# Optimization experiments

Measured on AMD Instinct MI355X. Metric: run time of the kernel, lower is better.

## Reference

```python
import jax, jax.numpy as jnp
import numpy as np

N_EXPERTS = 16
IN_DIM = 1024
OUT_DIM = 1024
BATCH = 4096

def setup_inputs() -> dict:
    key = jax.random.key(0)
    k1, k2, k3, k4 = jax.random.split(key, 4)
    x = jax.random.normal(k1, (BATCH, IN_DIM), dtype=jnp.float32)
    comp_weight = jax.random.uniform(k2, (BATCH, N_EXPERTS), dtype=jnp.float32)
    # torch.rand init (uniform [0,1)) per original module
    weight = jax.random.uniform(k3, (N_EXPERTS, IN_DIM, OUT_DIM), dtype=jnp.float32)
    bias = jax.random.uniform(k4, (N_EXPERTS, OUT_DIM), dtype=jnp.float32)
    return {"x": x, "comp_weight": comp_weight, "weight": weight, "bias": bias}

def reference(x, comp_weight, weight, bias):
    # z[n,b,o] = x[b,i] @ weight[n,i,o] + bias[n,o]   (baddbmm)
    z = jnp.einsum('bi,nio->nbo', x, weight) + bias[:, None, :]
    # out[b,o] = sum_n comp_weight[b,n] * z[n,b,o]    (bmm combine)
    out = jnp.einsum('bn,nbo->bo', comp_weight, z)
    return jax.nn.relu(out)
```

## Files before the change

kernel.cpp:

```cpp
#include <hip/hip_runtime.h>
#include <hip/hip_bf16.h>
#include <cstdint>

#define BATCH   4096
#define IN_DIM  1024
#define OUT_DIM 1024
#define NEXP    16

typedef __bf16 bf16;
typedef __attribute__((ext_vector_type(8))) __bf16 bf16x8;
typedef __attribute__((ext_vector_type(4))) float  f32x4;

#define AS1 __attribute__((address_space(1)))
#define AS3 __attribute__((address_space(3)))

__device__ __forceinline__ void gld_lds16(const bf16* g, bf16* l) {
    __builtin_amdgcn_global_load_lds((const AS1 void*)g, (AS3 void*)l, 16, 0, 0);
}

__global__ __launch_bounds__(256) void convert_all(
        const float* __restrict__ x, const float* __restrict__ W,
        bf16* __restrict__ xt, bf16* __restrict__ wt) {
    __shared__ float Ls[64][65];
    int t = threadIdx.x;
    int bid = blockIdx.x;
    if (bid < 4096) {
        int nblk = bid >> 8, ne = (bid >> 4) & 15, ks = bid & 15;
        int kb = ne * 1024 + ks * 64;
        int n0 = nblk * 64;
#pragma unroll
        for (int r = 0; r < 4; r++) {
            int idx = r * 256 + t;
            int row = idx >> 4, c4 = (idx & 15) * 4;
            f32x4 v = *(const f32x4*)(W + (size_t)(kb + row) * OUT_DIM + n0 + c4);
#pragma unroll
            for (int j = 0; j < 4; j++) Ls[row][c4 + j] = v[j];
        }
        __syncthreads();
#pragma unroll
        for (int r = 0; r < 2; r++) {
            int c = r * 256 + t;
            int sub = c >> 6, l = c & 63;
            int lr = l & 15, lq = l >> 4;
            int kk = sub >> 2, wn = (sub >> 1) & 1, nt = sub & 1;
            int krow = kk * 32 + lq * 8;
            int col = wn * 32 + nt * 16 + lr;
            bf16x8 v;
#pragma unroll
            for (int j = 0; j < 8; j++) v[j] = (bf16)Ls[krow + j][col];
            *(bf16x8*)(wt + (size_t)bid * 4096 + c * 8) = v;
        }
    } else {
        int tile = bid - 4096;
        int mblk = tile >> 4, ks = tile & 15;
#pragma unroll
        for (int r = 0; r < 4; r++) {
            int q = r * 256 + t;
            int m_loc = q >> 3, sc = q & 7;
            int cc = sc ^ (m_loc & 7);
            const float* src = x + (size_t)(mblk * 128 + m_loc) * IN_DIM + ks * 64 + cc * 8;
            f32x4 a = *(const f32x4*)src;
            f32x4 b = *(const f32x4*)(src + 4);
            bf16x8 v;
#pragma unroll
            for (int j = 0; j < 4; j++) { v[j] = (bf16)a[j]; v[4 + j] = (bf16)b[j]; }
            *(bf16x8*)(xt + (size_t)tile * 8192 + q * 8) = v;
        }
    }
}

__global__ __launch_bounds__(256, 3) void moe_gemm(
        const float* __restrict__ cw, const float* __restrict__ bias,
        const bf16* __restrict__ xt, const bf16* __restrict__ wt,
        float* __restrict__ out) {
    int nblk = blockIdx.x;
    int mblk = blockIdx.y;
    int m0 = mblk * 128, n0 = nblk * 64;
    int t = threadIdx.x;
    int lane = t & 63, w = t >> 6;
    int wm = w >> 1, wn = w & 1;
    int lq = lane >> 4, lr = lane & 15;

    __shared__ bf16 As[128 * 64];
    __shared__ bf16 Bs[4][64 * 64];
    __shared__ float cwT[16 * 132];

#pragma unroll
    for (int r = 0; r < 2; r++) {
        int q = r * 256 + t;
        f32x4 v = *(const f32x4*)(cw + (size_t)m0 * NEXP + q * 4);
        int row = q >> 2, nb = (q & 3) * 4;
#pragma unroll
        for (int c2 = 0; c2 < 4; c2++) cwT[(nb + c2) * 132 + row] = v[c2];
    }

    const f32x4 fz = {0.f, 0.f, 0.f, 0.f};
    f32x4 acc[4][2];
#pragma unroll
    for (int mt = 0; mt < 4; mt++)
#pragma unroll
        for (int nt = 0; nt < 2; nt++) acc[mt][nt] = fz;

    int swz = lr & 7;
    int mrow[4];
#pragma unroll
    for (int mt = 0; mt < 4; mt++) mrow[mt] = (wm * 64 + mt * 16 + lr) * 64;

    const bf16* abase = xt + (size_t)(mblk * 16) * 8192;
    const bf16* bbase = wt + (size_t)nblk * (16 * 16 * 4096);

    for (int ks = 0; ks < 16; ks++) {
        const bf16* asrc = abase + (size_t)ks * 8192 + t * 8;
#pragma unroll
        for (int r = 0; r < 4; r++) gld_lds16(asrc + r * 2048, &As[r * 2048 + t * 8]);
        const bf16* b0 = bbase + (size_t)ks * 4096 + t * 8;
        gld_lds16(b0,        &Bs[0][t * 8]);
        gld_lds16(b0 + 2048, &Bs[0][2048 + t * 8]);
        const bf16* b1 = bbase + (size_t)(16 + ks) * 4096 + t * 8;
        gld_lds16(b1,        &Bs[1][t * 8]);
        gld_lds16(b1 + 2048, &Bs[1][2048 + t * 8]);
        __syncthreads();

        bf16x8 af[4][2];
#pragma unroll
        for (int kk = 0; kk < 2; kk++)
#pragma unroll
            for (int mt = 0; mt < 4; mt++)
                af[mt][kk] = *(const bf16x8*)&As[mrow[mt] + ((kk * 4 + lq) ^ swz) * 8];

#pragma unroll 2
        for (int s = 0; s < 8; s++) {
            int nbase = s * 2;
            if (s < 7) {
                const bf16* bn2 = bbase + (size_t)((nbase + 2) * 16 + ks) * 4096 + t * 8;
                bf16* bd2 = &Bs[(nbase + 2) & 3][t * 8];
                gld_lds16(bn2,        bd2);
                gld_lds16(bn2 + 2048, bd2 + 2048);
                const bf16* bn3 = bbase + (size_t)((nbase + 3) * 16 + ks) * 4096 + t * 8;
                bf16* bd3 = &Bs[(nbase + 3) & 3][t * 8];
                gld_lds16(bn3,        bd3);
                gld_lds16(bn3 + 2048, bd3 + 2048);
            }
#pragma unroll
            for (int e = 0; e < 2; e++) {
                int ne = nbase + e;
                bf16x8 bfr[2][2];
#pragma unroll
                for (int kk = 0; kk < 2; kk++)
#pragma unroll
                    for (int nt = 0; nt < 2; nt++)
                        bfr[kk][nt] = *(const bf16x8*)
                            &Bs[ne & 3][((kk * 2 + wn) * 2 + nt) * 512 + lane * 8];
                f32x4 sc[4];
#pragma unroll
                for (int mt = 0; mt < 4; mt++)
                    sc[mt] = *(const f32x4*)&cwT[ne * 132 + wm * 64 + mt * 16 + lq * 4];
#pragma unroll
                for (int mt = 0; mt < 4; mt++)
#pragma unroll
                    for (int nt = 0; nt < 2; nt++) {
                        f32x4 p = __builtin_amdgcn_mfma_f32_16x16x32_bf16(
                            af[mt][0], bfr[0][nt], fz, 0, 0, 0);
                        p = __builtin_amdgcn_mfma_f32_16x16x32_bf16(
                            af[mt][1], bfr[1][nt], p, 0, 0, 0);
                        acc[mt][nt] += sc[mt] * p;
                    }
            }
            __syncthreads();
        }
    }

    {
        bf16x8 acw[4];
#pragma unroll
        for (int mt = 0; mt < 4; mt++) {
            bf16x8 v;
#pragma unroll
            for (int j = 0; j < 8; j++) v[j] = (bf16)0.f;
            if (lq < 2) {
                int row = m0 + wm * 64 + mt * 16 + lr;
                f32x4 a = *(const f32x4*)(cw + (size_t)row * NEXP + lq * 8);
                f32x4 b = *(const f32x4*)(cw + (size_t)row * NEXP + lq * 8 + 4);
#pragma unroll
                for (int j = 0; j < 4; j++) { v[j] = (bf16)a[j]; v[4 + j] = (bf16)b[j]; }
            }
            acw[mt] = v;
        }
        bf16x8 bb[2];
#pragma unroll
        for (int nt = 0; nt < 2; nt++) {
            bf16x8 v;
#pragma unroll
            for (int j = 0; j < 8; j++) v[j] = (bf16)0.f;
            if (lq < 2) {
                int col = n0 + wn * 32 + nt * 16 + lr;
#pragma unroll
                for (int j = 0; j < 8; j++)
                    v[j] = (bf16)bias[(size_t)(lq * 8 + j) * OUT_DIM + col];
            }
            bb[nt] = v;
        }
#pragma unroll
        for (int mt = 0; mt < 4; mt++)
#pragma unroll
            for (int nt = 0; nt < 2; nt++)
                acc[mt][nt] = __builtin_amdgcn_mfma_f32_16x16x32_bf16(
                    acw[mt], bb[nt], acc[mt][nt], 0, 0, 0);
    }

#pragma unroll
    for (int mt = 0; mt < 4; mt++) {
        int row = m0 + wm * 64 + mt * 16 + lq * 4;
#pragma unroll
        for (int nt = 0; nt < 2; nt++) {
            int col = n0 + wn * 32 + nt * 16 + lr;
#pragma unroll
            for (int r2 = 0; r2 < 4; r2++) {
                float v = acc[mt][nt][r2];
                out[(size_t)(row + r2) * OUT_DIM + col] = v > 0.f ? v : 0.f;
            }
        }
    }
}

__global__ void fallback_kernel(const float* __restrict__ x, const float* __restrict__ cw,
                                const float* __restrict__ W, const float* __restrict__ bias,
                                float* __restrict__ out) {
    int o = blockIdx.x * 256 + threadIdx.x;
    int b = o >> 10, oc = o & 1023;
    const float* xr = x + (size_t)b * IN_DIM;
    float accv = 0.f;
    for (int n = 0; n < NEXP; n++) {
        const float* wr = W + (size_t)n * IN_DIM * OUT_DIM + oc;
        float z = 0.f;
        for (int i = 0; i < IN_DIM; i++) z += xr[i] * wr[(size_t)i * OUT_DIM];
        accv += cw[(size_t)b * NEXP + n] * (z + bias[n * OUT_DIM + oc]);
    }
    out[o] = accv > 0.f ? accv : 0.f;
}

extern "C" void kernel_launch(void* const* d_in, const int* in_sizes, int n_in,
                              void* d_out, int out_size, void* d_ws, size_t ws_size,
                              hipStream_t stream) {
    const float* x    = (const float*)d_in[0];
    const float* cw   = (const float*)d_in[1];
    const float* W    = (const float*)d_in[2];
    const float* bias = (const float*)d_in[3];
    float* out = (float*)d_out;

    const size_t wt_elems = (size_t)NEXP * IN_DIM * OUT_DIM;
    const size_t xt_elems = (size_t)BATCH * IN_DIM;
    if (ws_size < (wt_elems + xt_elems) * sizeof(bf16)) {
        fallback_kernel<<<(BATCH * OUT_DIM) / 256, 256, 0, stream>>>(x, cw, W, bias, out);
        return;
    }
    bf16* wt = (bf16*)d_ws;
    bf16* xt = wt + wt_elems;

    convert_all<<<4096 + 512, 256, 0, stream>>>(x, W, xt, wt);
    moe_gemm<<<dim3(16, 32), 256, 0, stream>>>(cw, bias, xt, wt, out);
}
```

Before: 260.2 us.

## Transpose MFMA operands so per-row expert scales live in registers

Swaps the A and B operands of the MFMA so each lane's accumulator holds one row and four consecutive columns. This lets the per-row gating weights be loaded once into registers as scalars, replacing the LDS-transposed cw table, and lets the output be written with 16-byte vector stores. The expert loop is fully unrolled and launch bounds drop to 2 waves per SIMD to give room for the 64 extra scale registers. The risk is lower occupancy and more code size from the full unroll.

```diff
diff --git a/kernel.cpp b/kernel.cpp
--- a/kernel.cpp
+++ b/kernel.cpp
@@ -69,7 +69,7 @@
     }
 }
 
-__global__ __launch_bounds__(256, 3) void moe_gemm(
+__global__ __launch_bounds__(256, 2) void moe_gemm(
         const float* __restrict__ cw, const float* __restrict__ bias,
         const bf16* __restrict__ xt, const bf16* __restrict__ wt,
         float* __restrict__ out) {
@@ -83,15 +83,13 @@
 
     __shared__ bf16 As[128 * 64];
     __shared__ bf16 Bs[4][64 * 64];
-    __shared__ float cwT[16 * 132];
-
-#pragma unroll
-    for (int r = 0; r < 2; r++) {
-        int q = r * 256 + t;
-        f32x4 v = *(const f32x4*)(cw + (size_t)m0 * NEXP + q * 4);
-        int row = q >> 2, nb = (q & 3) * 4;
-#pragma unroll
-        for (int c2 = 0; c2 < 4; c2++) cwT[(nb + c2) * 132 + row] = v[c2];
+
+    f32x4 sreg[4][4];
+#pragma unroll
+    for (int mt = 0; mt < 4; mt++) {
+        const f32x4* p = (const f32x4*)(cw + (size_t)(m0 + wm * 64 + mt * 16 + lr) * NEXP);
+#pragma unroll
+        for (int g = 0; g < 4; g++) sreg[mt][g] = p[g];
     }
 
     const f32x4 fz = {0.f, 0.f, 0.f, 0.f};
@@ -109,6 +107,7 @@
     const bf16* abase = xt + (size_t)(mblk * 16) * 8192;
     const bf16* bbase = wt + (size_t)nblk * (16 * 16 * 4096);
 
+#pragma unroll 1
     for (int ks = 0; ks < 16; ks++) {
         const bf16* asrc = abase + (size_t)ks * 8192 + t * 8;
 #pragma unroll
@@ -128,45 +127,38 @@
             for (int mt = 0; mt < 4; mt++)
                 af[mt][kk] = *(const bf16x8*)&As[mrow[mt] + ((kk * 4 + lq) ^ swz) * 8];
 
-#pragma unroll 2
-        for (int s = 0; s < 8; s++) {
-            int nbase = s * 2;
-            if (s < 7) {
-                const bf16* bn2 = bbase + (size_t)((nbase + 2) * 16 + ks) * 4096 + t * 8;
-                bf16* bd2 = &Bs[(nbase + 2) & 3][t * 8];
+#pragma unroll
+        for (int ne = 0; ne < 16; ne++) {
+            if ((ne & 1) == 0 && ne < 14) {
+                const bf16* bn2 = bbase + (size_t)((ne + 2) * 16 + ks) * 4096 + t * 8;
+                bf16* bd2 = &Bs[(ne + 2) & 3][t * 8];
                 gld_lds16(bn2,        bd2);
                 gld_lds16(bn2 + 2048, bd2 + 2048);
-                const bf16* bn3 = bbase + (size_t)((nbase + 3) * 16 + ks) * 4096 + t * 8;
-                bf16* bd3 = &Bs[(nbase + 3) & 3][t * 8];
+                const bf16* bn3 = bbase + (size_t)((ne + 3) * 16 + ks) * 4096 + t * 8;
+                bf16* bd3 = &Bs[(ne + 3) & 3][t * 8];
                 gld_lds16(bn3,        bd3);
                 gld_lds16(bn3 + 2048, bd3 + 2048);
             }
-#pragma unroll
-            for (int e = 0; e < 2; e++) {
-                int ne = nbase + e;
-                bf16x8 bfr[2][2];
-#pragma unroll
-                for (int kk = 0; kk < 2; kk++)
-#pragma unroll
-                    for (int nt = 0; nt < 2; nt++)
-                        bfr[kk][nt] = *(const bf16x8*)
-                            &Bs[ne & 3][((kk * 2 + wn) * 2 + nt) * 512 + lane * 8];
-                f32x4 sc[4];
-#pragma unroll
-                for (int mt = 0; mt < 4; mt++)
-                    sc[mt] = *(const f32x4*)&cwT[ne * 132 + wm * 64 + mt * 16 + lq * 4];
-#pragma unroll
-                for (int mt = 0; mt < 4; mt++)
-#pragma unroll
-                    for (int nt = 0; nt < 2; nt++) {
-                        f32x4 p = __builtin_amdgcn_mfma_f32_16x16x32_bf16(
-                            af[mt][0], bfr[0][nt], fz, 0, 0, 0);
-                        p = __builtin_amdgcn_mfma_f32_16x16x32_bf16(
-                            af[mt][1], bfr[1][nt], p, 0, 0, 0);
-                        acc[mt][nt] += sc[mt] * p;
-                    }
-            }
-            __syncthreads();
+            bf16x8 bfr[2][2];
+#pragma unroll
+            for (int kk = 0; kk < 2; kk++)
+#pragma unroll
+                for (int nt = 0; nt < 2; nt++)
+                    bfr[kk][nt] = *(const bf16x8*)
+                        &Bs[ne & 3][((kk * 2 + wn) * 2 + nt) * 512 + lane * 8];
+#pragma unroll
+            for (int mt = 0; mt < 4; mt++) {
+                float sv = sreg[mt][ne >> 2][ne & 3];
+#pragma unroll
+                for (int nt = 0; nt < 2; nt++) {
+                    f32x4 p = __builtin_amdgcn_mfma_f32_16x16x32_bf16(
+                        bfr[0][nt], af[mt][0], fz, 0, 0, 0);
+                    p = __builtin_amdgcn_mfma_f32_16x16x32_bf16(
+                        bfr[1][nt], af[mt][1], p, 0, 0, 0);
+                    acc[mt][nt] += sv * p;
+                }
+            }
+            if (ne & 1) __syncthreads();
         }
     }
 
@@ -205,20 +197,19 @@
 #pragma unroll
             for (int nt = 0; nt < 2; nt++)
                 acc[mt][nt] = __builtin_amdgcn_mfma_f32_16x16x32_bf16(
-                    acw[mt], bb[nt], acc[mt][nt], 0, 0, 0);
+                    bb[nt], acw[mt], acc[mt][nt], 0, 0, 0);
     }
 
 #pragma unroll
     for (int mt = 0; mt < 4; mt++) {
-        int row = m0 + wm * 64 + mt * 16 + lq * 4;
+        int row = m0 + wm * 64 + mt * 16 + lr;
 #pragma unroll
         for (int nt = 0; nt < 2; nt++) {
-            int col = n0 + wn * 32 + nt * 16 + lr;
-#pragma unroll
-            for (int r2 = 0; r2 < 4; r2++) {
-                float v = acc[mt][nt][r2];
-                out[(size_t)(row + r2) * OUT_DIM + col] = v > 0.f ? v : 0.f;
-            }
+            int col = n0 + wn * 32 + nt * 16 + lq * 4;
+            f32x4 v = acc[mt][nt];
+#pragma unroll
+            for (int r2 = 0; r2 < 4; r2++) v[r2] = v[r2] > 0.f ? v[r2] : 0.f;
+            *(f32x4*)(out + (size_t)row * OUT_DIM + col) = v;
         }
     }
 }
```

Result: slower. 364.5 us (+40.1%).
